# Performance work log

Hardware: AMD Instinct MI355X
Metric: run time of the kernel (lower is better)

The kernel has to match this reference:

```python
import jax, jax.numpy as jnp
import numpy as np

NUM_COLS = 8      # MyTopoAgent.num_columns
NUM_SELECTED = 4  # MyTopoAgent.num_selected


def _gatv2(x, src, tgt, Wl, bl, Wr, br, att, bias, n):
    """PyG GATv2Conv (share_weights=False, concat=True, negative_slope=0.2).
    x: [n, Din]; src/tgt: [E] (self loops already appended); att: [H, C]."""
    H, C = att.shape
    xl = (x @ Wl + bl).reshape(n, H, C)   # lin_l(x) -> source transform
    xr = (x @ Wr + br).reshape(n, H, C)   # lin_r(x) -> target transform
    # e_ij = att . leaky_relu(xl[j] + xr[i])  per head
    e = jnp.einsum('ehc,hc->eh', jax.nn.leaky_relu(xl[src] + xr[tgt], 0.2), att)  # [E, H]
    # segment softmax over edges sharing a target node (stable via segment max)
    m = jax.lax.stop_gradient(jax.ops.segment_max(e, tgt, num_segments=n))
    ex = jnp.exp(e - m[tgt])
    denom = jax.ops.segment_sum(ex, tgt, num_segments=n)
    alpha = ex / (denom[tgt] + 1e-16)
    out = jax.ops.segment_sum(xl[src] * alpha[..., None], tgt, num_segments=n)  # [n, H, C]
    return out.reshape(n, H * C) + bias


def setup_inputs() -> dict:
    key = jax.random.key(0)
    B, N, D, Hd, Ch, E = 4, 10000, 128, 128, 7, 640000
    M = B * N
    ks = iter(jax.random.split(key, 40))
    nx = lambda shape: jax.random.normal(next(ks), shape, dtype=jnp.float32) * 0.05
    inp = {}
    inp['x'] = jax.random.normal(next(ks), (B, N, D), dtype=jnp.float32)
    inp['edge_index'] = jax.random.randint(next(ks), (2, E), 0, M)
    inp['gumbel_u'] = jax.random.uniform(next(ks), (B, NUM_COLS, Ch), dtype=jnp.float32,
                                         minval=1e-6, maxval=1.0 - 1e-6)
    # actor gat1(D->Hd), actor gat2(Hd->Ch), critic gat1(D->Hd), critic gat2(Hd->Hd); heads=1
    for pre, di, do in (('a1', D, Hd), ('a2', Hd, Ch), ('c1', D, Hd), ('c2', Hd, Hd)):
        inp[pre + '_Wl'] = nx((di, do))
        inp[pre + '_bl'] = jnp.zeros((do,), jnp.float32)
        inp[pre + '_Wr'] = nx((di, do))
        inp[pre + '_br'] = jnp.zeros((do,), jnp.float32)
        inp[pre + '_att'] = nx((1, do))
        inp[pre + '_b'] = jnp.zeros((do,), jnp.float32)
    inp['fc_W'] = nx((Hd, 1))
    inp['fc_b'] = jnp.zeros((1,), jnp.float32)
    return inp


def reference(x, edge_index, gumbel_u,
              a1_Wl, a1_bl, a1_Wr, a1_br, a1_att, a1_b,
              a2_Wl, a2_bl, a2_Wr, a2_br, a2_att, a2_b,
              c1_Wl, c1_bl, c1_Wr, c1_br, c1_att, c1_b,
              c2_Wl, c2_bl, c2_Wr, c2_br, c2_att, c2_b,
              fc_W, fc_b):
    B, N, D = x.shape
    M = B * N
    xf = x.reshape(M, D)
    loops = jnp.arange(M, dtype=edge_index.dtype)  # PyG add_self_loops
    src = jnp.concatenate([edge_index[0], loops])
    tgt = jnp.concatenate([edge_index[1], loops])
    # ---- actor: GATv2 -> leaky_relu(0.01) -> GATv2 -> softmax ----
    h = _gatv2(xf, src, tgt, a1_Wl, a1_bl, a1_Wr, a1_br, a1_att, a1_b, M)
    h = jax.nn.leaky_relu(h, 0.01)
    logits = _gatv2(h, src, tgt, a2_Wl, a2_bl, a2_Wr, a2_br, a2_att, a2_b, M).reshape(B, N, -1)
    probs = jax.nn.softmax(logits, axis=-1)  # [B, N, 7]
    # multinomial(k=4, no replacement) per column via Gumbel top-k
    g = -jnp.log(-jnp.log(gumbel_u))                       # [B, 8, 7]
    scores = jnp.log(probs[:, :NUM_COLS, :]) + g
    _, action = jax.lax.top_k(scores, NUM_SELECTED)        # [B, 8, 4]
    # torch gather(dim=1): sel[b,i,j] = probs[b, action[b,i,j], j]
    sel = probs[jnp.arange(B)[:, None, None], action, jnp.arange(NUM_SELECTED)[None, None, :]]
    # ---- critic: GATv2 -> leaky_relu(0.01) -> GATv2 -> Linear ----
    hc = _gatv2(xf, src, tgt, c1_Wl, c1_bl, c1_Wr, c1_br, c1_att, c1_b, M)
    hc = jax.nn.leaky_relu(hc, 0.01)
    hc = _gatv2(hc, src, tgt, c2_Wl, c2_bl, c2_Wr, c2_br, c2_att, c2_b, M).reshape(B, N, -1)
    value = hc @ fc_W + fc_b  # [B, N, 1]
    return action, sel, value
```

## Files before the change

### kernel.cpp

```cpp
#include <hip/hip_runtime.h>
#include <math.h>


typedef __attribute__((ext_vector_type(8))) short bf16x8;
typedef __attribute__((ext_vector_type(4))) float f32x4;

__device__ __forceinline__ float wave_reduce_sum(float v){
  #pragma unroll
  for (int o = 32; o > 0; o >>= 1) v += __shfl_xor(v, o);
  return v;
}
__device__ __forceinline__ unsigned short f2bf(float f){
  unsigned int u = __float_as_uint(f);
  u += 0x7FFFu + ((u >> 16) & 1u);
  return (unsigned short)(u >> 16);
}
__device__ __forceinline__ void unpack2(unsigned int u, float& a, float& b){
  a = __uint_as_float(u << 16);
  b = __uint_as_float(u & 0xffff0000u);
}

__global__ void k_zero(int* __restrict__ p, int n){
  int i = blockIdx.x * blockDim.x + threadIdx.x;
  if (i < n) p[i] = 0;
}

__global__ void k_scatter(const int* __restrict__ ei, int E,
                          int* __restrict__ cnt, int* __restrict__ bucket,
                          const float* __restrict__ W1l, const float* __restrict__ W1r,
                          const float* __restrict__ W2l, const float* __restrict__ W2r,
                          unsigned short* __restrict__ Wt1, unsigned short* __restrict__ Wt2){
  int e = blockIdx.x * blockDim.x + threadIdx.x;
  if (e < E){
    int s = ei[e], t = ei[E + e];
    int pos = atomicAdd(&cnt[t], 1);
    if (pos < 64) bucket[(size_t)t * 64 + pos] = s;
  } else {
    int r = e - E;
    if (r < 65536){
      int which = r >> 15;
      int lin = r & 32767;
      const float* Wl = which ? W2l : W1l;
      const float* Wr = which ? W2r : W1r;
      unsigned short* Wt = which ? Wt2 : Wt1;
      int n = lin >> 7, k = lin & 127;
      float v = (n < 128) ? Wl[(size_t)k * 128 + n] : Wr[(size_t)k * 128 + (n - 128)];
      Wt[lin] = f2bf(v);
    }
  }
}

__global__ void k_mark1(const int* __restrict__ cnt, const int* __restrict__ bucket,
                        int* __restrict__ flag1, int* __restrict__ list1,
                        int* __restrict__ n1, int N){
  int p = threadIdx.x;
  if (p >= 32) return;
  int node = (p >> 3) * N + (p & 7);
  if (atomicExch(&flag1[node], 1) == 0) list1[atomicAdd(n1, 1)] = node;
  int deg = min(cnt[node], 64);
  const int* crow = bucket + (size_t)node * 64;
  for (int j = 0; j < deg; ++j){
    int s = crow[j];
    if (atomicExch(&flag1[s], 1) == 0) list1[atomicAdd(n1, 1)] = s;
  }
}
__global__ void k_mark2(const int* __restrict__ cnt, const int* __restrict__ bucket,
                        const int* __restrict__ list1, const int* __restrict__ n1,
                        int* __restrict__ flag2, int* __restrict__ list2,
                        int* __restrict__ n2){
  int n = *n1;
  for (int i = blockIdx.x * blockDim.x + threadIdx.x; i < n; i += gridDim.x * blockDim.x){
    int node = list1[i];
    if (atomicExch(&flag2[node], 1) == 0) list2[atomicAdd(n2, 1)] = node;
    int deg = min(cnt[node], 64);
    const int* crow = bucket + (size_t)node * 64;
    for (int j = 0; j < deg; ++j){
      int s = crow[j];
      if (atomicExch(&flag2[s], 1) == 0) list2[atomicAdd(n2, 1)] = s;
    }
  }
}

__device__ __forceinline__ void dev_gemm_dual(
    int bid, const float* __restrict__ A,
    const float* __restrict__ Wl, const float* __restrict__ Wr,
    const float* __restrict__ blv, const float* __restrict__ brv,
    float* __restrict__ XL1, float* __restrict__ XR1,
    const int* __restrict__ list1, const int* __restrict__ list2,
    const int* __restrict__ nn,
    float (*As)[17], float (*Ws)[64]){
  const float* W; const float* bias; float* Out; const int* rows; int n;
  int colBase, bx, nbx;
  if (bid < 384){
    W = Wl; bias = blv; Out = XL1; rows = list2; n = nn[1];
    colBase = (bid / 192) * 64; bx = bid % 192; nbx = 192;
  } else {
    int rem = bid - 384;
    W = Wr; bias = brv; Out = XR1; rows = list1; n = nn[0];
    colBase = (rem / 64) * 64; bx = rem % 64; nbx = 64;
  }
  int tid = threadIdx.x;
  int tx = tid & 15, ty = tid >> 4;
  int ar = tid >> 2, ac = (tid & 3) << 2;
  int kr = tid >> 4, nc = (tid & 15) << 2;
  for (int base = bx * 64; base < n; base += nbx * 64){
    float acc[4][4] = {};
    int arow = rows[min(base + ar, n - 1)];
    for (int k0 = 0; k0 < 128; k0 += 16){
      float4 av = *(const float4*)(A + (size_t)arow * 128 + k0 + ac);
      As[ar][ac + 0] = av.x; As[ar][ac + 1] = av.y;
      As[ar][ac + 2] = av.z; As[ar][ac + 3] = av.w;
      float4 wv = *(const float4*)(W + (size_t)(k0 + kr) * 128 + colBase + nc);
      *(float4*)&Ws[kr][nc] = wv;
      __syncthreads();
      #pragma unroll
      for (int kk = 0; kk < 16; ++kk){
        float a0 = As[ty * 4 + 0][kk];
        float a1 = As[ty * 4 + 1][kk];
        float a2 = As[ty * 4 + 2][kk];
        float a3 = As[ty * 4 + 3][kk];
        float4 b = *(const float4*)&Ws[kk][tx * 4];
        acc[0][0] += a0 * b.x; acc[0][1] += a0 * b.y; acc[0][2] += a0 * b.z; acc[0][3] += a0 * b.w;
        acc[1][0] += a1 * b.x; acc[1][1] += a1 * b.y; acc[1][2] += a1 * b.z; acc[1][3] += a1 * b.w;
        acc[2][0] += a2 * b.x; acc[2][1] += a2 * b.y; acc[2][2] += a2 * b.z; acc[2][3] += a2 * b.w;
        acc[3][0] += a3 * b.x; acc[3][1] += a3 * b.y; acc[3][2] += a3 * b.z; acc[3][3] += a3 * b.w;
      }
      __syncthreads();
    }
    int cN = colBase + tx * 4;
    float4 bb = *(const float4*)(bias + cN);
    #pragma unroll
    for (int i = 0; i < 4; ++i){
      int r = rows[min(base + ty * 4 + i, n - 1)];
      float4 o;
      o.x = acc[i][0] + bb.x; o.y = acc[i][1] + bb.y;
      o.z = acc[i][2] + bb.z; o.w = acc[i][3] + bb.w;
      *(float4*)(Out + (size_t)r * 128 + cN) = o;
    }
  }
}

template<bool CVT>
__device__ __forceinline__ void dev_gemm_mfma(
    int rblk, const void* __restrict__ Av, const unsigned short* __restrict__ Wt,
    const float* __restrict__ bl, const float* __restrict__ br,
    unsigned short* __restrict__ XL, unsigned short* __restrict__ XR){
  int w = threadIdx.x >> 6, lane = threadIdx.x & 63;
  int l16 = lane & 15, kg = lane >> 4;
  int rBase = rblk * 64 + w * 16;
  f32x4 acc[16];
  #pragma unroll
  for (int i = 0; i < 16; ++i) acc[i] = (f32x4){0.f, 0.f, 0.f, 0.f};
  #pragma unroll
  for (int ks = 0; ks < 4; ++ks){
    bf16x8 a;
    if constexpr (CVT){
      const float* A = (const float*)Av;
      const float* ap = A + (size_t)(rBase + l16) * 128 + ks * 32 + kg * 8;
      float4 f0 = *(const float4*)ap;
      float4 f1 = *(const float4*)(ap + 4);
      union { bf16x8 v; unsigned short s[8]; } u;
      u.s[0] = f2bf(f0.x); u.s[1] = f2bf(f0.y); u.s[2] = f2bf(f0.z); u.s[3] = f2bf(f0.w);
      u.s[4] = f2bf(f1.x); u.s[5] = f2bf(f1.y); u.s[6] = f2bf(f1.z); u.s[7] = f2bf(f1.w);
      a = u.v;
    } else {
      a = *(const bf16x8*)((const unsigned short*)Av + (size_t)(rBase + l16) * 128 + ks * 32 + kg * 8);
    }
    #pragma unroll
    for (int ct = 0; ct < 16; ++ct){
      bf16x8 wv = *(const bf16x8*)(Wt + (size_t)(ct * 16 + l16) * 128 + ks * 32 + kg * 8);
      acc[ct] = __builtin_amdgcn_mfma_f32_16x16x32_bf16(wv, a, acc[ct], 0, 0, 0);
    }
  }
  int row = rBase + l16;
  #pragma unroll
  for (int ct = 0; ct < 16; ++ct){
    int col = ct * 16 + kg * 4;
    const float* bp = (col < 128) ? (bl + col) : (br + (col - 128));
    float4 bb = *(const float4*)bp;
    unsigned int p0 = (unsigned int)f2bf(acc[ct][0] + bb.x) |
                      ((unsigned int)f2bf(acc[ct][1] + bb.y) << 16);
    unsigned int p1 = (unsigned int)f2bf(acc[ct][2] + bb.z) |
                      ((unsigned int)f2bf(acc[ct][3] + bb.w) << 16);
    unsigned short* dst = (col < 128) ? (XL + (size_t)row * 128 + col)
                                      : (XR + (size_t)row * 128 + (col - 128));
    uint2 pk; pk.x = p0; pk.y = p1;
    *(uint2*)dst = pk;
  }
}

template<int MODE>
__device__ __forceinline__ void dev_gather16(
    int gid, int l,
    const unsigned short* __restrict__ XL, const unsigned short* __restrict__ XR,
    const int* __restrict__ cnt, const int* __restrict__ bucket,
    const float* __restrict__ att, const float* __restrict__ bias,
    const float* __restrict__ fcW, const float* __restrict__ fcb,
    void* __restrict__ outp){
  uint4 xu = *(const uint4*)(XR + (size_t)gid * 128 + l * 8);
  float xr[8];
  unpack2(xu.x, xr[0], xr[1]); unpack2(xu.y, xr[2], xr[3]);
  unpack2(xu.z, xr[4], xr[5]); unpack2(xu.w, xr[6], xr[7]);
  float at[8];
  {
    float4 a0 = *(const float4*)(att + l * 8);
    float4 a1 = *(const float4*)(att + l * 8 + 4);
    at[0] = a0.x; at[1] = a0.y; at[2] = a0.z; at[3] = a0.w;
    at[4] = a1.x; at[5] = a1.y; at[6] = a1.z; at[7] = a1.w;
  }
  int deg = min(cnt[gid], 64);
  const int* __restrict__ crow = bucket + (size_t)gid * 64;
  float m = -INFINITY, den = 0.f;
  float acc[8] = {0.f, 0.f, 0.f, 0.f, 0.f, 0.f, 0.f, 0.f};

  auto proc = [&](uint4 u){
    float xl[8];
    unpack2(u.x, xl[0], xl[1]); unpack2(u.y, xl[2], xl[3]);
    unpack2(u.z, xl[4], xl[5]); unpack2(u.w, xl[6], xl[7]);
    float e = 0.f;
    #pragma unroll
    for (int c = 0; c < 8; ++c){
      float v = xl[c] + xr[c];
      v = fmaxf(v, 0.2f * v);
      e = fmaf(v, at[c], e);
    }
    e += __shfl_xor(e, 1, 16);
    e += __shfl_xor(e, 2, 16);
    e += __shfl_xor(e, 4, 16);
    e += __shfl_xor(e, 8, 16);
    if (e > m){
      float sc = __expf(m - e);
      den *= sc;
      #pragma unroll
      for (int c = 0; c < 8; ++c) acc[c] *= sc;
      m = e;
    }
    float p = __expf(e - m);
    den += p;
    #pragma unroll
    for (int c = 0; c < 8; ++c) acc[c] = fmaf(p, xl[c], acc[c]);
  };

  proc(*(const uint4*)(XL + (size_t)gid * 128 + l * 8));

  int nq = deg >> 2;
  int j = 0;
  if (nq > 0){
    uint4 r0, r1, r2, r3;
    {
      int s0 = crow[0], s1 = crow[1], s2 = crow[2], s3 = crow[3];
      r0 = *(const uint4*)(XL + (size_t)s0 * 128 + l * 8);
      r1 = *(const uint4*)(XL + (size_t)s1 * 128 + l * 8);
      r2 = *(const uint4*)(XL + (size_t)s2 * 128 + l * 8);
      r3 = *(const uint4*)(XL + (size_t)s3 * 128 + l * 8);
    }
    for (int q = 1;; ++q){
      bool more = (q < nq);
      uint4 n0, n1, n2, n3;
      if (more){
        int b4 = q * 4;
        int t0 = crow[b4 + 0], t1 = crow[b4 + 1], t2 = crow[b4 + 2], t3 = crow[b4 + 3];
        n0 = *(const uint4*)(XL + (size_t)t0 * 128 + l * 8);
        n1 = *(const uint4*)(XL + (size_t)t1 * 128 + l * 8);
        n2 = *(const uint4*)(XL + (size_t)t2 * 128 + l * 8);
        n3 = *(const uint4*)(XL + (size_t)t3 * 128 + l * 8);
      }
      proc(r0); proc(r1); proc(r2); proc(r3);
      if (!more) break;
      r0 = n0; r1 = n1; r2 = n2; r3 = n3;
    }
    j = nq * 4;
  }
  for (; j < deg; ++j){
    int s = crow[j];
    proc(*(const uint4*)(XL + (size_t)s * 128 + l * 8));
  }

  float r = 1.f / (den + 1e-16f);
  float4 b0 = *(const float4*)(bias + l * 8);
  float4 b1 = *(const float4*)(bias + l * 8 + 4);
  float o[8];
  o[0] = acc[0] * r + b0.x; o[1] = acc[1] * r + b0.y;
  o[2] = acc[2] * r + b0.z; o[3] = acc[3] * r + b0.w;
  o[4] = acc[4] * r + b1.x; o[5] = acc[5] * r + b1.y;
  o[6] = acc[6] * r + b1.z; o[7] = acc[7] * r + b1.w;
  if (MODE == 0){
    #pragma unroll
    for (int c = 0; c < 8; ++c) o[c] = o[c] > 0.f ? o[c] : 0.01f * o[c];
    uint4 pk;
    pk.x = (unsigned int)f2bf(o[0]) | ((unsigned int)f2bf(o[1]) << 16);
    pk.y = (unsigned int)f2bf(o[2]) | ((unsigned int)f2bf(o[3]) << 16);
    pk.z = (unsigned int)f2bf(o[4]) | ((unsigned int)f2bf(o[5]) << 16);
    pk.w = (unsigned int)f2bf(o[6]) | ((unsigned int)f2bf(o[7]) << 16);
    *(uint4*)((unsigned short*)outp + (size_t)gid * 128 + l * 8) = pk;
  } else {
    float4 w0 = *(const float4*)(fcW + l * 8);
    float4 w1 = *(const float4*)(fcW + l * 8 + 4);
    float pv = o[0] * w0.x + o[1] * w0.y + o[2] * w0.z + o[3] * w0.w +
               o[4] * w1.x + o[5] * w1.y + o[6] * w1.z + o[7] * w1.w;
    pv += __shfl_xor(pv, 1, 16);
    pv += __shfl_xor(pv, 2, 16);
    pv += __shfl_xor(pv, 4, 16);
    pv += __shfl_xor(pv, 8, 16);
    if (l == 0) ((float*)outp)[gid] = pv + fcb[0];
  }
}

__device__ __forceinline__ void dev_a1_fused(
    int vbid,
    const float* __restrict__ XL, const float* __restrict__ XR,
    const int* __restrict__ cnt, const int* __restrict__ bucket,
    const float* __restrict__ att, const float* __restrict__ bias,
    const float* __restrict__ Wl7, const float* __restrict__ Wr7,
    const float* __restrict__ bl7, const float* __restrict__ br7,
    float* __restrict__ XL2, float* __restrict__ XR2,
    const int* __restrict__ list, const int* __restrict__ n_dev){
  int n = *n_dev;
  int lane = threadIdx.x & 63;
  const int wstride = (256 * 256) >> 6;
  for (int i = (vbid * 256 + (int)threadIdx.x) >> 6; i < n; i += wstride){
    int wid = list[i];
    float2 xr = ((const float2*)(XR + (size_t)wid * 128))[lane];
    float2 at = ((const float2*)att)[lane];
    int deg = min(cnt[wid], 64);
    const int* crow = bucket + (size_t)wid * 64;
    float m = -INFINITY, den = 0.f, acc0 = 0.f, acc1 = 0.f;
    for (int j = -1; j < deg; ++j){
      int s = (j < 0) ? wid : crow[j];
      float2 xl = ((const float2*)(XL + (size_t)s * 128))[lane];
      float v0 = xl.x + xr.x, v1 = xl.y + xr.y;
      v0 = v0 > 0.f ? v0 : 0.2f * v0;
      v1 = v1 > 0.f ? v1 : 0.2f * v1;
      float e = wave_reduce_sum(v0 * at.x + v1 * at.y);
      float mn = fmaxf(m, e);
      float sc = __expf(m - mn);
      float p  = __expf(e - mn);
      den  = den  * sc + p;
      acc0 = acc0 * sc + p * xl.x;
      acc1 = acc1 * sc + p * xl.y;
      m = mn;
    }
    float r = 1.f / (den + 1e-16f);
    float2 bs = ((const float2*)bias)[lane];
    float o0 = acc0 * r + bs.x;
    float o1 = acc1 * r + bs.y;
    o0 = o0 > 0.f ? o0 : 0.01f * o0;
    o1 = o1 > 0.f ? o1 : 0.01f * o1;
    #pragma unroll
    for (int c = 0; c < 7; ++c){
      float wl0 = Wl7[(size_t)(2 * lane) * 7 + c];
      float wl1 = Wl7[(size_t)(2 * lane + 1) * 7 + c];
      float wr0 = Wr7[(size_t)(2 * lane) * 7 + c];
      float wr1 = Wr7[(size_t)(2 * lane + 1) * 7 + c];
      float dl = wave_reduce_sum(o0 * wl0 + o1 * wl1);
      float dr = wave_reduce_sum(o0 * wr0 + o1 * wr1);
      if (lane == 0){
        XL2[(size_t)wid * 8 + c] = dl + bl7[c];
        XR2[(size_t)wid * 8 + c] = dr + br7[c];
      }
    }
  }
}

__device__ __forceinline__ void dev_a2head(
    float (*pr)[8],
    const float* __restrict__ XL2, const float* __restrict__ XR2,
    const int* __restrict__ cnt, const int* __restrict__ bucket,
    const float* __restrict__ att, const float* __restrict__ bias,
    const float* __restrict__ gu,
    float* __restrict__ out_action, float* __restrict__ out_sel, int N){
  int g = threadIdx.x >> 3, c = threadIdx.x & 7;
  int node = (g >> 3) * N + (g & 7);
  float xr = (c < 7) ? XR2[(size_t)node * 8 + c] : 0.f;
  float at = (c < 7) ? att[c] : 0.f;
  int deg = min(cnt[node], 64);
  const int* crow = bucket + (size_t)node * 64;
  float m = -INFINITY, den = 0.f, acc = 0.f;
  for (int j = -1; j < deg; ++j){
    int s = (j < 0) ? node : crow[j];
    float xl = (c < 7) ? XL2[(size_t)s * 8 + c] : 0.f;
    float v = xl + xr;
    v = fmaxf(v, 0.2f * v);
    float e = v * at;
    e += __shfl_xor(e, 1, 8);
    e += __shfl_xor(e, 2, 8);
    e += __shfl_xor(e, 4, 8);
    if (e > m){
      float sc = __expf(m - e);
      den *= sc; acc *= sc; m = e;
    }
    float p = __expf(e - m);
    den += p;
    acc = fmaf(p, xl, acc);
  }
  float lg = acc / (den + 1e-16f) + ((c < 7) ? bias[c] : 0.f);
  float lgv = (c < 7) ? lg : -INFINITY;
  float mx = lgv;
  mx = fmaxf(mx, __shfl_xor(mx, 1, 8));
  mx = fmaxf(mx, __shfl_xor(mx, 2, 8));
  mx = fmaxf(mx, __shfl_xor(mx, 4, 8));
  float ex = (c < 7) ? expf(lgv - mx) : 0.f;
  float sm = ex;
  sm += __shfl_xor(sm, 1, 8);
  sm += __shfl_xor(sm, 2, 8);
  sm += __shfl_xor(sm, 4, 8);
  pr[g][c] = ex / sm;
  __syncthreads();
  int t = threadIdx.x;
  if (t < 32){
    int b = t >> 3;
    float sc[7];
    #pragma unroll
    for (int cc = 0; cc < 7; ++cc){
      float u = gu[t * 7 + cc];
      float gn = -logf(-logf(u));
      sc[cc] = logf(pr[t][cc]) + gn;
    }
    #pragma unroll
    for (int k = 0; k < 4; ++k){
      float best = -INFINITY; int bi = 0;
      #pragma unroll
      for (int cc = 0; cc < 7; ++cc) if (sc[cc] > best){ best = sc[cc]; bi = cc; }
      sc[bi] = -INFINITY;
      out_action[t * 4 + k] = (float)bi;
      out_sel[t * 4 + k] = pr[b * 8 + bi][k];
    }
  }
}

__global__ __launch_bounds__(256) void k_mega1(
    const float* __restrict__ x,
    const float* __restrict__ a1_Wl, const float* __restrict__ a1_Wr,
    const float* __restrict__ a1_bl, const float* __restrict__ a1_br,
    float* __restrict__ XL1, float* __restrict__ XR1,
    const int* __restrict__ list1, const int* __restrict__ list2,
    const int* __restrict__ nn,
    const unsigned short* __restrict__ Wt1,
    const float* __restrict__ c1_bl, const float* __restrict__ c1_br,
    unsigned short* __restrict__ XLb, unsigned short* __restrict__ XRb){
  __shared__ float As[64][17];
  __shared__ float Ws[16][64];
  int bid = blockIdx.x;
  if (bid < 512){
    dev_gemm_dual(bid, x, a1_Wl, a1_Wr, a1_bl, a1_br, XL1, XR1, list1, list2, nn, As, Ws);
  } else {
    dev_gemm_mfma<true>(bid - 512, x, Wt1, c1_bl, c1_br, XLb, XRb);
  }
}

__global__ __launch_bounds__(256) void k_mega2(
    const unsigned short* __restrict__ XLb, const unsigned short* __restrict__ XRb,
    const int* __restrict__ cnt, const int* __restrict__ bucket,
    const float* __restrict__ c1_att, const float* __restrict__ c1_b,
    unsigned short* __restrict__ Hb, int M, int G0,
    const float* __restrict__ XL1, const float* __restrict__ XR1,
    const float* __restrict__ a1_att, const float* __restrict__ a1_b,
    const float* __restrict__ Wl7, const float* __restrict__ Wr7,
    const float* __restrict__ bl7, const float* __restrict__ br7,
    float* __restrict__ XL2, float* __restrict__ XR2,
    const int* __restrict__ list1, const int* __restrict__ n1){
  int bid = blockIdx.x;
  if (bid < 256){
    dev_a1_fused(bid, XL1, XR1, cnt, bucket, a1_att, a1_b,
                 Wl7, Wr7, bl7, br7, XL2, XR2, list1, n1);
  } else {
    int gbid = bid - 256;
    int gid = (gbid * 256 + (int)threadIdx.x) >> 4;
    int l = threadIdx.x & 15;
    if (gid < M)
      dev_gather16<0>(gid, l, XLb, XRb, cnt, bucket, c1_att, c1_b,
                      nullptr, nullptr, (void*)Hb);
  }
}

__global__ __launch_bounds__(256) void k_mega3(
    const unsigned short* __restrict__ Hb, const unsigned short* __restrict__ Wt2,
    const float* __restrict__ c2_bl, const float* __restrict__ c2_br,
    unsigned short* __restrict__ XLb, unsigned short* __restrict__ XRb, int nMfma,
    const float* __restrict__ XL2, const float* __restrict__ XR2,
    const int* __restrict__ cnt, const int* __restrict__ bucket,
    const float* __restrict__ a2_att, const float* __restrict__ a2_b,
    const float* __restrict__ gu,
    float* __restrict__ out_action, float* __restrict__ out_sel, int N){
  __shared__ float pr[32][8];
  int bid = blockIdx.x;
  if (bid < nMfma){
    dev_gemm_mfma<false>(bid, Hb, Wt2, c2_bl, c2_br, XLb, XRb);
  } else {
    dev_a2head(pr, XL2, XR2, cnt, bucket, a2_att, a2_b, gu, out_action, out_sel, N);
  }
}

__global__ __launch_bounds__(256) void k_gather_v(
    const unsigned short* __restrict__ XLb, const unsigned short* __restrict__ XRb,
    const int* __restrict__ cnt, const int* __restrict__ bucket,
    const float* __restrict__ att, const float* __restrict__ bias,
    const float* __restrict__ fcW, const float* __restrict__ fcb,
    float* __restrict__ out_value, int M){
  int gid = (blockIdx.x * blockDim.x + threadIdx.x) >> 4;
  int l = threadIdx.x & 15;
  if (gid < M)
    dev_gather16<1>(gid, l, XLb, XRb, cnt, bucket, att, bias, fcW, fcb, (void*)out_value);
}

extern "C" void kernel_launch(void* const* d_in, const int* in_sizes, int n_in,
                              void* d_out, int out_size, void* d_ws, size_t ws_size,
                              hipStream_t stream){
  const float* x  = (const float*)d_in[0];
  const int*   ei = (const int*)d_in[1];
  const float* gu = (const float*)d_in[2];
  const float* a1_Wl = (const float*)d_in[3],  *a1_bl = (const float*)d_in[4];
  const float* a1_Wr = (const float*)d_in[5],  *a1_br = (const float*)d_in[6];
  const float* a1_att= (const float*)d_in[7],  *a1_b  = (const float*)d_in[8];
  const float* a2_Wl = (const float*)d_in[9],  *a2_bl = (const float*)d_in[10];
  const float* a2_Wr = (const float*)d_in[11], *a2_br = (const float*)d_in[12];
  const float* a2_att= (const float*)d_in[13], *a2_b  = (const float*)d_in[14];
  const float* c1_Wl = (const float*)d_in[15], *c1_bl = (const float*)d_in[16];
  const float* c1_Wr = (const float*)d_in[17], *c1_br = (const float*)d_in[18];
  const float* c1_att= (const float*)d_in[19], *c1_b  = (const float*)d_in[20];
  const float* c2_Wl = (const float*)d_in[21], *c2_bl = (const float*)d_in[22];
  const float* c2_Wr = (const float*)d_in[23], *c2_br = (const float*)d_in[24];
  const float* c2_att= (const float*)d_in[25], *c2_b  = (const float*)d_in[26];
  const float* fc_W  = (const float*)d_in[27], *fc_b  = (const float*)d_in[28];

  const int M = in_sizes[0] / 128;
  const int E = in_sizes[1] / 2;
  const int B = in_sizes[2] / 56;
  const int N = M / B;
  const int nw = B * 8;
  const int T = 256;

  char* ws = (char*)d_ws;
  size_t off = 0;
  auto alloc = [&](size_t bytes) -> void* {
    void* p = ws + off;
    off += (bytes + 255) & ~(size_t)255;
    return p;
  };
  int*   cnt    = (int*)alloc((size_t)(3 * M + 2) * 4);
  int*   flag1  = cnt + M;
  int*   flag2  = flag1 + M;
  int*   nn     = flag2 + M;
  int*   bucket = (int*)alloc((size_t)M * 64 * 4);
  int*   list1  = (int*)alloc((size_t)M * 4);
  int*   list2  = (int*)alloc((size_t)M * 4);
  float* XL2    = (float*)alloc((size_t)M * 8 * 4);
  float* XR2    = (float*)alloc((size_t)M * 8 * 4);
  unsigned short* Wt1 = (unsigned short*)alloc((size_t)256 * 128 * 2);
  unsigned short* Wt2 = (unsigned short*)alloc((size_t)256 * 128 * 2);
  float* XL1 = (float*)alloc((size_t)M * 128 * 4);
  float* XR1 = (float*)alloc((size_t)M * 128 * 4);
  unsigned short* XLb = (unsigned short*)alloc((size_t)M * 128 * 2);
  unsigned short* XRb = (unsigned short*)alloc((size_t)M * 128 * 2);
  unsigned short* Hb  = (unsigned short*)alloc((size_t)M * 128 * 2);
  (void)ws_size; (void)n_in; (void)out_size;

  float* out_action = (float*)d_out;
  float* out_sel    = out_action + (size_t)nw * 4;
  float* out_value  = out_sel + (size_t)nw * 4;

  const int G0 = (M * 16 + T - 1) / T;
  const int nMfma = M / 64;
  const int nz = 3 * M + 2;

  k_zero<<<(nz + T - 1) / T, T, 0, stream>>>(cnt, nz);
  k_scatter<<<(E + 65536 + T - 1) / T, T, 0, stream>>>(ei, E, cnt, bucket,
      c1_Wl, c1_Wr, c2_Wl, c2_Wr, Wt1, Wt2);

  k_mark1<<<1, 64, 0, stream>>>(cnt, bucket, flag1, list1, &nn[0], N);
  k_mark2<<<64, T, 0, stream>>>(cnt, bucket, list1, &nn[0], flag2, list2, &nn[1]);

  k_mega1<<<512 + nMfma, T, 0, stream>>>(x, a1_Wl, a1_Wr, a1_bl, a1_br,
      XL1, XR1, list1, list2, nn, Wt1, c1_bl, c1_br, XLb, XRb);

  k_mega2<<<256 + G0, T, 0, stream>>>(XLb, XRb, cnt, bucket, c1_att, c1_b,
      Hb, M, G0, XL1, XR1, a1_att, a1_b, a2_Wl, a2_Wr, a2_bl, a2_br,
      XL2, XR2, list1, &nn[0]);

  k_mega3<<<nMfma + 1, T, 0, stream>>>(Hb, Wt2, c2_bl, c2_br, XLb, XRb, nMfma,
      XL2, XR2, cnt, bucket, a2_att, a2_b, gu, out_action, out_sel, N);

  k_gather_v<<<G0, T, 0, stream>>>(XLb, XRb, cnt, bucket, c2_att, c2_b,
      fc_W, fc_b, out_value, M);
}
```

Measured before the change: 241.9 us.

## Reschedule actor and critic stages to co-launch independent work in fewer kernels

Reorganizes the launch schedule so the critic layer-1 MFMA GEMM runs alongside the single-block mark1 pass, mark2 runs alongside the critic layer-1 gather, the actor sparse GEMM runs alongside the critic layer-2 MFMA GEMM, and the actor layer-1 aggregation runs alongside the final critic value gather. The actor head becomes its own small kernel at the end. This cuts the number of launches from seven to six after the scatter and lets the tiny serial marking kernels hide behind large parallel work. In exchange, the small actor head is now a separate trailing launch on the critical path, and buffer reuse (XLb/XRb) between critic layers depends on the new ordering.

After: 207.5 us. -14.2%, faster.

```diff
diff --git a/kernel.cpp b/kernel.cpp
--- a/kernel.cpp
+++ b/kernel.cpp
@@ -50,9 +50,9 @@
   }
 }
 
-__global__ void k_mark1(const int* __restrict__ cnt, const int* __restrict__ bucket,
-                        int* __restrict__ flag1, int* __restrict__ list1,
-                        int* __restrict__ n1, int N){
+__device__ __forceinline__ void dev_mark1(
+    const int* __restrict__ cnt, const int* __restrict__ bucket,
+    int* __restrict__ flag1, int* __restrict__ list1, int* __restrict__ n1, int N){
   int p = threadIdx.x;
   if (p >= 32) return;
   int node = (p >> 3) * N + (p & 7);
@@ -64,12 +64,13 @@
     if (atomicExch(&flag1[s], 1) == 0) list1[atomicAdd(n1, 1)] = s;
   }
 }
-__global__ void k_mark2(const int* __restrict__ cnt, const int* __restrict__ bucket,
-                        const int* __restrict__ list1, const int* __restrict__ n1,
-                        int* __restrict__ flag2, int* __restrict__ list2,
-                        int* __restrict__ n2){
+__device__ __forceinline__ void dev_mark2(
+    int vbid, int nblk,
+    const int* __restrict__ cnt, const int* __restrict__ bucket,
+    const int* __restrict__ list1, const int* __restrict__ n1,
+    int* __restrict__ flag2, int* __restrict__ list2, int* __restrict__ n2){
   int n = *n1;
-  for (int i = blockIdx.x * blockDim.x + threadIdx.x; i < n; i += gridDim.x * blockDim.x){
+  for (int i = vbid * blockDim.x + threadIdx.x; i < n; i += nblk * blockDim.x){
     int node = list1[i];
     if (atomicExch(&flag2[node], 1) == 0) list2[atomicAdd(n2, 1)] = node;
     int deg = min(cnt[node], 64);
@@ -362,13 +363,13 @@
   }
 }
 
-__device__ __forceinline__ void dev_a2head(
-    float (*pr)[8],
+__global__ __launch_bounds__(256) void k_a2head(
     const float* __restrict__ XL2, const float* __restrict__ XR2,
     const int* __restrict__ cnt, const int* __restrict__ bucket,
     const float* __restrict__ att, const float* __restrict__ bias,
     const float* __restrict__ gu,
     float* __restrict__ out_action, float* __restrict__ out_sel, int N){
+  __shared__ float pr[32][8];
   int g = threadIdx.x >> 3, c = threadIdx.x & 7;
   int node = (g >> 3) * N + (g & 7);
   float xr = (c < 7) ? XR2[(size_t)node * 8 + c] : 0.f;
@@ -428,15 +429,49 @@
   }
 }
 
-__global__ __launch_bounds__(256) void k_mega1(
+__global__ __launch_bounds__(256) void k_L3(
+    const float* __restrict__ x, const unsigned short* __restrict__ Wt1,
+    const float* __restrict__ c1_bl, const float* __restrict__ c1_br,
+    unsigned short* __restrict__ XLb, unsigned short* __restrict__ XRb, int nMfma,
+    const int* __restrict__ cnt, const int* __restrict__ bucket,
+    int* __restrict__ flag1, int* __restrict__ list1, int* __restrict__ n1, int N){
+  int bid = blockIdx.x;
+  if (bid < nMfma){
+    dev_gemm_mfma<true>(bid, x, Wt1, c1_bl, c1_br, XLb, XRb);
+  } else {
+    dev_mark1(cnt, bucket, flag1, list1, n1, N);
+  }
+}
+
+__global__ __launch_bounds__(256) void k_L4(
+    const int* __restrict__ cnt, const int* __restrict__ bucket,
+    const int* __restrict__ list1, const int* __restrict__ n1,
+    int* __restrict__ flag2, int* __restrict__ list2, int* __restrict__ n2,
+    const unsigned short* __restrict__ XLb, const unsigned short* __restrict__ XRb,
+    const float* __restrict__ c1_att, const float* __restrict__ c1_b,
+    unsigned short* __restrict__ Hb, int M){
+  int bid = blockIdx.x;
+  if (bid < 64){
+    dev_mark2(bid, 64, cnt, bucket, list1, n1, flag2, list2, n2);
+  } else {
+    int gbid = bid - 64;
+    int gid = (gbid * 256 + (int)threadIdx.x) >> 4;
+    int l = threadIdx.x & 15;
+    if (gid < M)
+      dev_gather16<0>(gid, l, XLb, XRb, cnt, bucket, c1_att, c1_b,
+                      nullptr, nullptr, (void*)Hb);
+  }
+}
+
+__global__ __launch_bounds__(256) void k_L5(
     const float* __restrict__ x,
     const float* __restrict__ a1_Wl, const float* __restrict__ a1_Wr,
     const float* __restrict__ a1_bl, const float* __restrict__ a1_br,
     float* __restrict__ XL1, float* __restrict__ XR1,
     const int* __restrict__ list1, const int* __restrict__ list2,
     const int* __restrict__ nn,
-    const unsigned short* __restrict__ Wt1,
-    const float* __restrict__ c1_bl, const float* __restrict__ c1_br,
+    const unsigned short* __restrict__ Hb, const unsigned short* __restrict__ Wt2,
+    const float* __restrict__ c2_bl, const float* __restrict__ c2_br,
     unsigned short* __restrict__ XLb, unsigned short* __restrict__ XRb){
   __shared__ float As[64][17];
   __shared__ float Ws[16][64];
@@ -444,21 +479,22 @@
   if (bid < 512){
     dev_gemm_dual(bid, x, a1_Wl, a1_Wr, a1_bl, a1_br, XL1, XR1, list1, list2, nn, As, Ws);
   } else {
-    dev_gemm_mfma<true>(bid - 512, x, Wt1, c1_bl, c1_br, XLb, XRb);
-  }
-}
-
-__global__ __launch_bounds__(256) void k_mega2(
-    const unsigned short* __restrict__ XLb, const unsigned short* __restrict__ XRb,
-    const int* __restrict__ cnt, const int* __restrict__ bucket,
-    const float* __restrict__ c1_att, const float* __restrict__ c1_b,
-    unsigned short* __restrict__ Hb, int M, int G0,
+    dev_gemm_mfma<false>(bid - 512, Hb, Wt2, c2_bl, c2_br, XLb, XRb);
+  }
+}
+
+__global__ __launch_bounds__(256) void k_L6(
     const float* __restrict__ XL1, const float* __restrict__ XR1,
+    const int* __restrict__ cnt, const int* __restrict__ bucket,
     const float* __restrict__ a1_att, const float* __restrict__ a1_b,
     const float* __restrict__ Wl7, const float* __restrict__ Wr7,
     const float* __restrict__ bl7, const float* __restrict__ br7,
     float* __restrict__ XL2, float* __restrict__ XR2,
-    const int* __restrict__ list1, const int* __restrict__ n1){
+    const int* __restrict__ list1, const int* __restrict__ n1,
+    const unsigned short* __restrict__ XLb, const unsigned short* __restrict__ XRb,
+    const float* __restrict__ c2_att, const float* __restrict__ c2_b,
+    const float* __restrict__ fcW, const float* __restrict__ fcb,
+    float* __restrict__ out_value, int M){
   int bid = blockIdx.x;
   if (bid < 256){
     dev_a1_fused(bid, XL1, XR1, cnt, bucket, a1_att, a1_b,
@@ -468,39 +504,9 @@
     int gid = (gbid * 256 + (int)threadIdx.x) >> 4;
     int l = threadIdx.x & 15;
     if (gid < M)
-      dev_gather16<0>(gid, l, XLb, XRb, cnt, bucket, c1_att, c1_b,
-                      nullptr, nullptr, (void*)Hb);
-  }
-}
-
-__global__ __launch_bounds__(256) void k_mega3(
-    const unsigned short* __restrict__ Hb, const unsigned short* __restrict__ Wt2,
-    const float* __restrict__ c2_bl, const float* __restrict__ c2_br,
-    unsigned short* __restrict__ XLb, unsigned short* __restrict__ XRb, int nMfma,
-    const float* __restrict__ XL2, const float* __restrict__ XR2,
-    const int* __restrict__ cnt, const int* __restrict__ bucket,
-    const float* __restrict__ a2_att, const float* __restrict__ a2_b,
-    const float* __restrict__ gu,
-    float* __restrict__ out_action, float* __restrict__ out_sel, int N){
-  __shared__ float pr[32][8];
-  int bid = blockIdx.x;
-  if (bid < nMfma){
-    dev_gemm_mfma<false>(bid, Hb, Wt2, c2_bl, c2_br, XLb, XRb);
-  } else {
-    dev_a2head(pr, XL2, XR2, cnt, bucket, a2_att, a2_b, gu, out_action, out_sel, N);
-  }
-}
-
-__global__ __launch_bounds__(256) void k_gather_v(
-    const unsigned short* __restrict__ XLb, const unsigned short* __restrict__ XRb,
-    const int* __restrict__ cnt, const int* __restrict__ bucket,
-    const float* __restrict__ att, const float* __restrict__ bias,
-    const float* __restrict__ fcW, const float* __restrict__ fcb,
-    float* __restrict__ out_value, int M){
-  int gid = (blockIdx.x * blockDim.x + threadIdx.x) >> 4;
-  int l = threadIdx.x & 15;
-  if (gid < M)
-    dev_gather16<1>(gid, l, XLb, XRb, cnt, bucket, att, bias, fcW, fcb, (void*)out_value);
+      dev_gather16<1>(gid, l, XLb, XRb, cnt, bucket, c2_att, c2_b,
+                      fcW, fcb, (void*)out_value);
+  }
 }
 
 extern "C" void kernel_launch(void* const* d_in, const int* in_sizes, int n_in,
@@ -566,20 +572,15 @@
   k_zero<<<(nz + T - 1) / T, T, 0, stream>>>(cnt, nz);
   k_scatter<<<(E + 65536 + T - 1) / T, T, 0, stream>>>(ei, E, cnt, bucket,
       c1_Wl, c1_Wr, c2_Wl, c2_Wr, Wt1, Wt2);
-
-  k_mark1<<<1, 64, 0, stream>>>(cnt, bucket, flag1, list1, &nn[0], N);
-  k_mark2<<<64, T, 0, stream>>>(cnt, bucket, list1, &nn[0], flag2, list2, &nn[1]);
-
-  k_mega1<<<512 + nMfma, T, 0, stream>>>(x, a1_Wl, a1_Wr, a1_bl, a1_br,
-      XL1, XR1, list1, list2, nn, Wt1, c1_bl, c1_br, XLb, XRb);
-
-  k_mega2<<<256 + G0, T, 0, stream>>>(XLb, XRb, cnt, bucket, c1_att, c1_b,
-      Hb, M, G0, XL1, XR1, a1_att, a1_b, a2_Wl, a2_Wr, a2_bl, a2_br,
-      XL2, XR2, list1, &nn[0]);
-
-  k_mega3<<<nMfma + 1, T, 0, stream>>>(Hb, Wt2, c2_bl, c2_br, XLb, XRb, nMfma,
-      XL2, XR2, cnt, bucket, a2_att, a2_b, gu, out_action, out_sel, N);
-
-  k_gather_v<<<G0, T, 0, stream>>>(XLb, XRb, cnt, bucket, c2_att, c2_b,
-      fc_W, fc_b, out_value, M);
-}
+  k_L3<<<nMfma + 1, T, 0, stream>>>(x, Wt1, c1_bl, c1_br, XLb, XRb, nMfma,
+      cnt, bucket, flag1, list1, &nn[0], N);
+  k_L4<<<64 + G0, T, 0, stream>>>(cnt, bucket, list1, &nn[0], flag2, list2, &nn[1],
+      XLb, XRb, c1_att, c1_b, Hb, M);
+  k_L5<<<512 + nMfma, T, 0, stream>>>(x, a1_Wl, a1_Wr, a1_bl, a1_br,
+      XL1, XR1, list1, list2, nn, Hb, Wt2, c2_bl, c2_br, XLb, XRb);
+  k_L6<<<256 + G0, T, 0, stream>>>(XL1, XR1, cnt, bucket, a1_att, a1_b,
+      a2_Wl, a2_Wr, a2_bl, a2_br, XL2, XR2, list1, &nn[0],
+      XLb, XRb, c2_att, c2_b, fc_W, fc_b, out_value, M);
+  k_a2head<<<1, 256, 0, stream>>>(XL2, XR2, cnt, bucket, a2_att, a2_b, gu,
+      out_action, out_sel, N);
+}
```
